# Performance work log

Measured on AMD Instinct MI355X. Metric: run time of the kernel, lower is better.

Reference implementation:

```python
import jax, jax.numpy as jnp
import numpy as np

M_POS = 0.5
M_NEG_SIM = 0.1
LAM_NEG = 1.0


def setup_inputs() -> dict:
    key = jax.random.key(0)
    N, d, G = 8192, 1024, 64
    codebook = jax.random.normal(key, (N, d), dtype=jnp.float32)
    base = (jnp.arange(N) // G) * G  # contiguous groups of size G (vq_to_range)
    starts = base.astype(jnp.int32)
    ends = (base + G - 1).astype(jnp.int32)
    return {"codebook": codebook, "starts": starts, "ends": ends, "max_i": N - 1}


def reference(codebook, starts, ends, max_i):
    N, d = codebook.shape
    M = min(N, int(max_i) + 1)  # rows processed by the python loop

    # cosine similarity rows [0:M] vs all N
    zn = codebook / jnp.linalg.norm(codebook, axis=-1, keepdims=True)
    cos = jnp.einsum('md,nd->mn', zn[:M], zn)  # (M, N)

    # pairwise Euclidean distances rows [0:M] vs all N via ||a-b||^2 = |a|^2+|b|^2-2ab
    sq = jnp.sum(codebook * codebook, axis=-1)  # (N,)
    dot = jnp.einsum('md,nd->mn', codebook[:M], codebook)  # (M, N)
    d2 = jnp.maximum(sq[:M, None] + sq[None, :] - 2.0 * dot, 0.0)

    j = jnp.arange(N)[None, :]
    i = jnp.arange(M)[:, None]
    in_range = (j >= starts[:M, None]) & (j <= ends[:M, None])
    pos_mask = in_range & (j != i)
    # original: group_mask[i]=False then neg = ~group_mask, so i is in negatives
    neg_mask = (~in_range) | (j == i)

    pos_cnt = jnp.sum(pos_mask, axis=-1)
    neg_cnt = jnp.sum(neg_mask, axis=-1)

    # safe sqrt: only evaluate on positive-mask entries
    D = jnp.sqrt(jnp.where(pos_mask, d2, 1.0))
    pos_term = jnp.square(jax.nn.relu(D - M_POS)) * pos_mask
    pos_pull = jnp.sum(pos_term, axis=-1) / jnp.maximum(pos_cnt, 1)

    neg_cos = jnp.clip(cos, -1.0, 1.0)
    neg_term = jnp.square(jax.nn.relu(jnp.abs(neg_cos) - M_NEG_SIM)) * neg_mask
    ortho = jnp.sum(neg_term, axis=-1) / jnp.maximum(neg_cnt, 1)

    valid = (pos_cnt > 0) & (neg_cnt > 0)
    per_row = jnp.where(valid, pos_pull + LAM_NEG * ortho, 0.0)
    cnt = jnp.sum(valid)
    total = jnp.sum(per_row)
    return jnp.where(cnt > 0, total / jnp.maximum(cnt, 1).astype(total.dtype), jnp.zeros((), total.dtype))
```

## Files before the change

kernel.cpp:

```cpp
#include <hip/hip_runtime.h>
#include <hip/hip_bf16.h>
#include <stdint.h>

#define M_POS 0.5f
#define M_NEG 0.1f
#define LAM_NEG 1.0f

typedef __attribute__((ext_vector_type(4))) float floatx4;
typedef __attribute__((ext_vector_type(8))) int   intx8;

union Frag8 { intx8 v; int4 q[2]; };

__global__ __launch_bounds__(256) void prep_kernel(
    const float* __restrict__ cb, unsigned char* __restrict__ cb_q,
    float* __restrict__ sq, float* __restrict__ inv_norm,
    unsigned* __restrict__ zero_base, int zero_len,
    int N, int d)
{
    const int gi = blockIdx.x * 256 + threadIdx.x;
    if (gi < zero_len) zero_base[gi] = 0u;

    const int row = blockIdx.x;
    const float* src = cb + (size_t)row * d;
    unsigned char* dst = cb_q + (size_t)row * d;
    const int t = threadIdx.x;

    float s = 0.f;
    for (int c = t * 4; c < d; c += 1024) {
        float4 v = *(const float4*)(src + c);
        s += v.x * v.x + v.y * v.y + v.z * v.z + v.w * v.w;
        int pk = __builtin_amdgcn_cvt_pk_fp8_f32(v.x, v.y, 0, false);
        pk     = __builtin_amdgcn_cvt_pk_fp8_f32(v.z, v.w, pk, true);
        *(int*)(dst + c) = pk;
    }
    for (int o = 32; o > 0; o >>= 1) s += __shfl_down(s, o, 64);
    __shared__ float wsum[4];
    if ((t & 63) == 0) wsum[t >> 6] = s;
    __syncthreads();
    if (t == 0) {
        float tot = wsum[0] + wsum[1] + wsum[2] + wsum[3];
        sq[row] = tot;
        inv_norm[row] = rsqrtf(tot);
    }
}

__global__ __launch_bounds__(256, 3) void gram_loss_kernel(
    const unsigned char* __restrict__ A,
    const float* __restrict__ sq, const float* __restrict__ inv_norm,
    const int* __restrict__ starts, const int* __restrict__ ends,
    const int* __restrict__ max_ip,
    float* __restrict__ pos_acc, float* __restrict__ neg_acc,
    unsigned* __restrict__ counter, float* __restrict__ out,
    int N, int d)
{
    const int M = min(N, max_ip[0] + 1);

    int vt = blockIdx.x;
    const int nB = gridDim.x;
    if ((nB & 7) == 0) {
        const int per = nB >> 3;
        vt = (blockIdx.x & 7) * per + (blockIdx.x >> 3);
    }

    int bx = (int)((sqrtf(8.f * (float)vt + 1.f) - 1.f) * 0.5f);
    while ((bx + 1) * (bx + 2) / 2 <= vt) bx++;
    while (bx * (bx + 1) / 2 > vt) bx--;
    const int by = vt - bx * (bx + 1) / 2;

    const int rowBase = by * 128;
    const int colBase = bx * 128;
    const bool isDiag = (by == bx);

    __shared__ alignas(16) unsigned char ldsA[128 * 128];
    __shared__ alignas(16) unsigned char ldsB[128 * 128];

    const int tid  = threadIdx.x;
    const int wave = tid >> 6;
    const int lane = tid & 63;
    const int wr = (wave >> 1) * 64;
    const int wc = (wave & 1) * 64;

    floatx4 acc[4][4];
#pragma unroll
    for (int a = 0; a < 4; ++a)
#pragma unroll
        for (int b = 0; b < 4; ++b) acc[a][b] = (floatx4){0.f, 0.f, 0.f, 0.f};

    const int sRow = lane >> 3;
    const int sChk = lane & 7;
    const int srcOffC = ((sChk ^ sRow) * 16);
    const int kTiles = d / 128;

    const int rl = lane & 15;
    const int g  = lane >> 4;
    const int rx = rl & 7;
    const int c0 = (((2 * g)     ^ rx) * 16);
    const int c1 = (((2 * g + 1) ^ rx) * 16);

    for (int kt = 0; kt < kTiles; ++kt) {
        __syncthreads();
        const int k0 = kt * 128;
#pragma unroll
        for (int h = 0; h < 4; ++h) {
            const int r = wave * 32 + h * 8 + sRow;
            const unsigned char* ga = A + (size_t)(rowBase + r) * d + k0 + srcOffC;
            const unsigned char* gb = A + (size_t)(colBase + r) * d + k0 + srcOffC;
            __builtin_amdgcn_global_load_lds(
                (const __attribute__((address_space(1))) void*)ga,
                (__attribute__((address_space(3))) void*)(ldsA + r * 128 + sChk * 16), 16, 0, 0);
            __builtin_amdgcn_global_load_lds(
                (const __attribute__((address_space(1))) void*)gb,
                (__attribute__((address_space(3))) void*)(ldsB + r * 128 + sChk * 16), 16, 0, 0);
        }
        __syncthreads();

        Frag8 af[4], bf[4];
#pragma unroll
        for (int t4 = 0; t4 < 4; ++t4) {
            const unsigned char* pa = ldsA + (wr + t4 * 16 + rl) * 128;
            af[t4].q[0] = *(const int4*)(pa + c0);
            af[t4].q[1] = *(const int4*)(pa + c1);
            const unsigned char* pb = ldsB + (wc + t4 * 16 + rl) * 128;
            bf[t4].q[0] = *(const int4*)(pb + c0);
            bf[t4].q[1] = *(const int4*)(pb + c1);
        }
#pragma unroll
        for (int rt = 0; rt < 4; ++rt)
#pragma unroll
            for (int ct = 0; ct < 4; ++ct)
                acc[rt][ct] = __builtin_amdgcn_mfma_scale_f32_16x16x128_f8f6f4(
                    af[rt].v, bf[ct].v, acc[rt][ct], 0, 0, 0, 127, 0, 127);
    }

    const int q  = lane >> 4;
    const int jlo = colBase + wc;
    const int ilo = rowBase + wr;

    int   jn[4];
    float jinv[4];
    bool  jvalid[4];
#pragma unroll
    for (int ct = 0; ct < 4; ++ct) {
        const int j = jlo + ct * 16 + rl;
        jn[ct]  = j;
        jinv[ct] = inv_norm[j];
        jvalid[ct] = (j < M);
    }

    bool posLane = false;
    {
        const int ri = ilo + lane;
        if (ri < M) posLane |= (ends[ri] >= jlo) && (starts[ri] <= jlo + 63);
        if (!isDiag) {
            const int cj = jlo + lane;
            if (cj < M) posLane |= (ends[cj] >= ilo) && (starts[cj] <= ilo + 63);
        }
    }
    const bool fullPath = (__ballot(posLane) != 0ULL);

    float posc[4] = {0.f, 0.f, 0.f, 0.f};
    float negc[4] = {0.f, 0.f, 0.f, 0.f};

    if (fullPath) {
        int   jns[4], jne[4];
        float jsq[4];
#pragma unroll
        for (int ct = 0; ct < 4; ++ct) {
            jsq[ct] = sq[jn[ct]];
            jns[ct] = jvalid[ct] ? starts[jn[ct]] : 0;
            jne[ct] = jvalid[ct] ? ends[jn[ct]]   : -1;
        }
#pragma unroll
        for (int rt = 0; rt < 4; ++rt) {
            const int ibase = ilo + rt * 16 + q * 4;
#pragma unroll
            for (int reg = 0; reg < 4; ++reg) {
                const int i = ibase + reg;
                const bool rowValid = (i < M);
                const int ns = rowValid ? starts[i] : 0;
                const int ne = rowValid ? ends[i]   : -1;
                const float iinv = inv_norm[i];
                const float isq  = sq[i];
                float posp = 0.f, negp = 0.f;
#pragma unroll
                for (int ct = 0; ct < 4; ++ct) {
                    const float dot = acc[rt][ct][reg];
                    const int j = jn[ct];
                    float cosv = dot * iinv * jinv[ct];
                    cosv = fminf(fmaxf(cosv, -1.f), 1.f);
                    float tn = fmaxf(fabsf(cosv) - M_NEG, 0.f);
                    const float nterm = tn * tn;
                    const float d2 = fmaxf(isq + jsq[ct] - 2.f * dot, 0.f);
                    float tp = fmaxf(sqrtf(d2) - M_POS, 0.f);
                    const float pterm = tp * tp;
                    const bool dg = (j == i);
                    if (rowValid) {
                        const bool in_r = (j >= ns) && (j <= ne);
                        if (in_r && !dg) posp += pterm;
                        if (!in_r || dg) negp += nterm;
                    }
                    if (!isDiag && jvalid[ct]) {
                        const bool in_c = (i >= jns[ct]) && (i <= jne[ct]);
                        if (in_c && !dg) posc[ct] += pterm;
                        if (!in_c || dg) negc[ct] += nterm;
                    }
                }
#pragma unroll
                for (int m = 1; m < 16; m <<= 1) {
                    posp += __shfl_xor(posp, m, 64);
                    negp += __shfl_xor(negp, m, 64);
                }
                if (rowValid && rl == 0) {
                    atomicAdd(&pos_acc[i], posp);
                    atomicAdd(&neg_acc[i], negp);
                }
            }
        }
        if (!isDiag) {
#pragma unroll
            for (int ct = 0; ct < 4; ++ct) {
                posc[ct] += __shfl_xor(posc[ct], 16, 64);
                posc[ct] += __shfl_xor(posc[ct], 32, 64);
                negc[ct] += __shfl_xor(negc[ct], 16, 64);
                negc[ct] += __shfl_xor(negc[ct], 32, 64);
            }
            if (q == 0) {
#pragma unroll
                for (int ct = 0; ct < 4; ++ct) {
                    if (jvalid[ct]) {
                        atomicAdd(&pos_acc[jn[ct]], posc[ct]);
                        atomicAdd(&neg_acc[jn[ct]], negc[ct]);
                    }
                }
            }
        }
    } else {
#pragma unroll
        for (int rt = 0; rt < 4; ++rt) {
            const int ibase = ilo + rt * 16 + q * 4;
#pragma unroll
            for (int reg = 0; reg < 4; ++reg) {
                const int i = ibase + reg;
                const float iinv = inv_norm[i];
                float negp = 0.f;
#pragma unroll
                for (int ct = 0; ct < 4; ++ct) {
                    const float dot = acc[rt][ct][reg];
                    float cosv = dot * iinv * jinv[ct];
                    cosv = fminf(fmaxf(cosv, -1.f), 1.f);
                    float tn = fmaxf(fabsf(cosv) - M_NEG, 0.f);
                    const float nterm = tn * tn;
                    negp += nterm;
                    negc[ct] += nterm;
                }
#pragma unroll
                for (int m = 1; m < 16; m <<= 1)
                    negp += __shfl_xor(negp, m, 64);
                if ((i < M) && rl == 0)
                    atomicAdd(&neg_acc[i], negp);
            }
        }
        if (!isDiag) {
#pragma unroll
            for (int ct = 0; ct < 4; ++ct) {
                negc[ct] += __shfl_xor(negc[ct], 16, 64);
                negc[ct] += __shfl_xor(negc[ct], 32, 64);
            }
            if (q == 0) {
#pragma unroll
                for (int ct = 0; ct < 4; ++ct)
                    if (jvalid[ct])
                        atomicAdd(&neg_acc[jn[ct]], negc[ct]);
            }
        }
    }

    __shared__ bool amLast;
    __syncthreads();
    if (tid == 0) {
        __threadfence();
        unsigned old = atomicAdd(counter, 1u);
        amLast = (old == (unsigned)(gridDim.x - 1));
    }
    __syncthreads();
    if (amLast) {
        __threadfence();
        float total = 0.f;
        int cnt = 0;
        for (int i = tid; i < M; i += 256) {
            const float pa = __hip_atomic_load(&pos_acc[i], __ATOMIC_RELAXED, __HIP_MEMORY_SCOPE_AGENT);
            const float na = __hip_atomic_load(&neg_acc[i], __ATOMIC_RELAXED, __HIP_MEMORY_SCOPE_AGENT);
            const int ns = starts[i], ne = ends[i];
            const int lo = max(ns, 0), hi = min(ne, N - 1);
            const int inr = max(hi - lo + 1, 0);
            const bool dg = (i >= ns) && (i <= ne);
            const int pos_cnt = inr - (dg ? 1 : 0);
            const int neg_cnt = N - inr + (dg ? 1 : 0);
            if (pos_cnt > 0 && neg_cnt > 0) {
                total += pa / (float)max(pos_cnt, 1)
                       + LAM_NEG * na / (float)max(neg_cnt, 1);
                cnt++;
            }
        }
        for (int o = 32; o > 0; o >>= 1) {
            total += __shfl_down(total, o, 64);
            cnt   += __shfl_down(cnt, o, 64);
        }
        __shared__ float fin_ts[4];
        __shared__ int   fin_cs[4];
        if ((tid & 63) == 0) { fin_ts[tid >> 6] = total; fin_cs[tid >> 6] = cnt; }
        __syncthreads();
        if (tid == 0) {
            float T = fin_ts[0] + fin_ts[1] + fin_ts[2] + fin_ts[3];
            int   C = fin_cs[0] + fin_cs[1] + fin_cs[2] + fin_cs[3];
            out[0] = (C > 0) ? T / (float)C : 0.f;
        }
    }
}

extern "C" void kernel_launch(void* const* d_in, const int* in_sizes, int n_in,
                              void* d_out, int out_size, void* d_ws, size_t ws_size,
                              hipStream_t stream) {
    const float* cb     = (const float*)d_in[0];
    const int*   starts = (const int*)d_in[1];
    const int*   ends   = (const int*)d_in[2];
    const int*   max_ip = (const int*)d_in[3];
    float* out = (float*)d_out;

    const int N = in_sizes[1];
    const int d = in_sizes[0] / N;

    char* ws = (char*)d_ws;
    unsigned char* cb_q = (unsigned char*)ws;
    size_t off = ((size_t)N * d + 255) & ~(size_t)255;
    float* sq       = (float*)(ws + off); off += (size_t)N * 4;
    float* inv_norm = (float*)(ws + off); off += (size_t)N * 4;
    float* pos_acc  = (float*)(ws + off); off += (size_t)N * 4;
    float* neg_acc  = (float*)(ws + off); off += (size_t)N * 4;
    unsigned* counter = (unsigned*)(ws + off); off += 256;

    prep_kernel<<<N, 256, 0, stream>>>(cb, cb_q, sq, inv_norm,
                                       (unsigned*)pos_acc, 2 * N + 1, N, d);

    const int nb = N / 128;
    const int nBlocks = nb * (nb + 1) / 2;
    gram_loss_kernel<<<nBlocks, 256, 0, stream>>>(cb_q, sq, inv_norm, starts, ends,
                                                  max_ip, pos_acc, neg_acc, counter,
                                                  out, N, d);
}
```

Baseline: 196.9 us.

## Split each 128x128 Gram tile into two 128x64 column-half blocks

Each upper-triangular 128x128 tile is now split into two blocks, each computing a 128x64 half, which doubles the grid. The B LDS buffer, the MFMA accumulators and the epilogue loops shrink to match, and launch bounds rise to allow four blocks per CU. The aim is better occupancy and load balance through lower register and LDS use per block. In exchange, each A tile is loaded twice, so global/L2 traffic goes up and data reuse per block goes down.

```diff
diff --git a/kernel.cpp b/kernel.cpp
--- a/kernel.cpp
+++ b/kernel.cpp
@@ -44,7 +44,7 @@
     }
 }
 
-__global__ __launch_bounds__(256, 3) void gram_loss_kernel(
+__global__ __launch_bounds__(256, 4) void gram_loss_kernel(
     const unsigned char* __restrict__ A,
     const float* __restrict__ sq, const float* __restrict__ inv_norm,
     const int* __restrict__ starts, const int* __restrict__ ends,
@@ -62,29 +62,31 @@
         vt = (blockIdx.x & 7) * per + (blockIdx.x >> 3);
     }
 
-    int bx = (int)((sqrtf(8.f * (float)vt + 1.f) - 1.f) * 0.5f);
-    while ((bx + 1) * (bx + 2) / 2 <= vt) bx++;
-    while (bx * (bx + 1) / 2 > vt) bx--;
-    const int by = vt - bx * (bx + 1) / 2;
+    const int sqt  = vt >> 1;
+    const int half = vt & 1;
+    int bx = (int)((sqrtf(8.f * (float)sqt + 1.f) - 1.f) * 0.5f);
+    while ((bx + 1) * (bx + 2) / 2 <= sqt) bx++;
+    while (bx * (bx + 1) / 2 > sqt) bx--;
+    const int by = sqt - bx * (bx + 1) / 2;
 
     const int rowBase = by * 128;
-    const int colBase = bx * 128;
+    const int colBase = bx * 128 + half * 64;
     const bool isDiag = (by == bx);
 
     __shared__ alignas(16) unsigned char ldsA[128 * 128];
-    __shared__ alignas(16) unsigned char ldsB[128 * 128];
+    __shared__ alignas(16) unsigned char ldsB[64 * 128];
 
     const int tid  = threadIdx.x;
     const int wave = tid >> 6;
     const int lane = tid & 63;
     const int wr = (wave >> 1) * 64;
-    const int wc = (wave & 1) * 64;
-
-    floatx4 acc[4][4];
+    const int wc = (wave & 1) * 32;
+
+    floatx4 acc[4][2];
 #pragma unroll
     for (int a = 0; a < 4; ++a)
 #pragma unroll
-        for (int b = 0; b < 4; ++b) acc[a][b] = (floatx4){0.f, 0.f, 0.f, 0.f};
+        for (int b = 0; b < 2; ++b) acc[a][b] = (floatx4){0.f, 0.f, 0.f, 0.f};
 
     const int sRow = lane >> 3;
     const int sChk = lane & 7;
@@ -104,43 +106,50 @@
         for (int h = 0; h < 4; ++h) {
             const int r = wave * 32 + h * 8 + sRow;
             const unsigned char* ga = A + (size_t)(rowBase + r) * d + k0 + srcOffC;
-            const unsigned char* gb = A + (size_t)(colBase + r) * d + k0 + srcOffC;
             __builtin_amdgcn_global_load_lds(
                 (const __attribute__((address_space(1))) void*)ga,
                 (__attribute__((address_space(3))) void*)(ldsA + r * 128 + sChk * 16), 16, 0, 0);
+        }
+#pragma unroll
+        for (int h = 0; h < 2; ++h) {
+            const int r = wave * 16 + h * 8 + sRow;
+            const unsigned char* gb = A + (size_t)(colBase + r) * d + k0 + srcOffC;
             __builtin_amdgcn_global_load_lds(
                 (const __attribute__((address_space(1))) void*)gb,
                 (__attribute__((address_space(3))) void*)(ldsB + r * 128 + sChk * 16), 16, 0, 0);
         }
         __syncthreads();
 
-        Frag8 af[4], bf[4];
+        Frag8 af[4], bf[2];
 #pragma unroll
         for (int t4 = 0; t4 < 4; ++t4) {
             const unsigned char* pa = ldsA + (wr + t4 * 16 + rl) * 128;
             af[t4].q[0] = *(const int4*)(pa + c0);
             af[t4].q[1] = *(const int4*)(pa + c1);
-            const unsigned char* pb = ldsB + (wc + t4 * 16 + rl) * 128;
-            bf[t4].q[0] = *(const int4*)(pb + c0);
-            bf[t4].q[1] = *(const int4*)(pb + c1);
+        }
+#pragma unroll
+        for (int t2 = 0; t2 < 2; ++t2) {
+            const unsigned char* pb = ldsB + (wc + t2 * 16 + rl) * 128;
+            bf[t2].q[0] = *(const int4*)(pb + c0);
+            bf[t2].q[1] = *(const int4*)(pb + c1);
         }
 #pragma unroll
         for (int rt = 0; rt < 4; ++rt)
 #pragma unroll
-            for (int ct = 0; ct < 4; ++ct)
+            for (int ct = 0; ct < 2; ++ct)
                 acc[rt][ct] = __builtin_amdgcn_mfma_scale_f32_16x16x128_f8f6f4(
                     af[rt].v, bf[ct].v, acc[rt][ct], 0, 0, 0, 127, 0, 127);
     }
 
-    const int q  = lane >> 4;
+    const int q  = g;
     const int jlo = colBase + wc;
     const int ilo = rowBase + wr;
 
-    int   jn[4];
-    float jinv[4];
-    bool  jvalid[4];
-#pragma unroll
-    for (int ct = 0; ct < 4; ++ct) {
+    int   jn[2];
+    float jinv[2];
+    bool  jvalid[2];
+#pragma unroll
+    for (int ct = 0; ct < 2; ++ct) {
         const int j = jlo + ct * 16 + rl;
         jn[ct]  = j;
         jinv[ct] = inv_norm[j];
@@ -150,22 +159,22 @@
     bool posLane = false;
     {
         const int ri = ilo + lane;
-        if (ri < M) posLane |= (ends[ri] >= jlo) && (starts[ri] <= jlo + 63);
-        if (!isDiag) {
+        if (ri < M) posLane |= (ends[ri] >= jlo) && (starts[ri] <= jlo + 31);
+        if (!isDiag && lane < 32) {
             const int cj = jlo + lane;
             if (cj < M) posLane |= (ends[cj] >= ilo) && (starts[cj] <= ilo + 63);
         }
     }
     const bool fullPath = (__ballot(posLane) != 0ULL);
 
-    float posc[4] = {0.f, 0.f, 0.f, 0.f};
-    float negc[4] = {0.f, 0.f, 0.f, 0.f};
+    float posc[2] = {0.f, 0.f};
+    float negc[2] = {0.f, 0.f};
 
     if (fullPath) {
-        int   jns[4], jne[4];
-        float jsq[4];
-#pragma unroll
-        for (int ct = 0; ct < 4; ++ct) {
+        int   jns[2], jne[2];
+        float jsq[2];
+#pragma unroll
+        for (int ct = 0; ct < 2; ++ct) {
             jsq[ct] = sq[jn[ct]];
             jns[ct] = jvalid[ct] ? starts[jn[ct]] : 0;
             jne[ct] = jvalid[ct] ? ends[jn[ct]]   : -1;
@@ -183,7 +192,7 @@
                 const float isq  = sq[i];
                 float posp = 0.f, negp = 0.f;
 #pragma unroll
-                for (int ct = 0; ct < 4; ++ct) {
+                for (int ct = 0; ct < 2; ++ct) {
                     const float dot = acc[rt][ct][reg];
                     const int j = jn[ct];
                     float cosv = dot * iinv * jinv[ct];
@@ -218,7 +227,7 @@
         }
         if (!isDiag) {
 #pragma unroll
-            for (int ct = 0; ct < 4; ++ct) {
+            for (int ct = 0; ct < 2; ++ct) {
                 posc[ct] += __shfl_xor(posc[ct], 16, 64);
                 posc[ct] += __shfl_xor(posc[ct], 32, 64);
                 negc[ct] += __shfl_xor(negc[ct], 16, 64);
@@ -226,7 +235,7 @@
             }
             if (q == 0) {
 #pragma unroll
-                for (int ct = 0; ct < 4; ++ct) {
+                for (int ct = 0; ct < 2; ++ct) {
                     if (jvalid[ct]) {
                         atomicAdd(&pos_acc[jn[ct]], posc[ct]);
                         atomicAdd(&neg_acc[jn[ct]], negc[ct]);
@@ -244,7 +253,7 @@
                 const float iinv = inv_norm[i];
                 float negp = 0.f;
 #pragma unroll
-                for (int ct = 0; ct < 4; ++ct) {
+                for (int ct = 0; ct < 2; ++ct) {
                     const float dot = acc[rt][ct][reg];
                     float cosv = dot * iinv * jinv[ct];
                     cosv = fminf(fmaxf(cosv, -1.f), 1.f);
@@ -262,13 +271,13 @@
         }
         if (!isDiag) {
 #pragma unroll
-            for (int ct = 0; ct < 4; ++ct) {
+            for (int ct = 0; ct < 2; ++ct) {
                 negc[ct] += __shfl_xor(negc[ct], 16, 64);
                 negc[ct] += __shfl_xor(negc[ct], 32, 64);
             }
             if (q == 0) {
 #pragma unroll
-                for (int ct = 0; ct < 4; ++ct)
+                for (int ct = 0; ct < 2; ++ct)
                     if (jvalid[ct])
                         atomicAdd(&neg_acc[jn[ct]], negc[ct]);
             }
@@ -343,7 +352,8 @@
                                        (unsigned*)pos_acc, 2 * N + 1, N, d);
 
     const int nb = N / 128;
-    const int nBlocks = nb * (nb + 1) / 2;
+    const int nSquares = nb * (nb + 1) / 2;
+    const int nBlocks = nSquares * 2;
     gram_loss_kernel<<<nBlocks, 256, 0, stream>>>(cb_q, sq, inv_norm, starts, ends,
                                                   max_ip, pos_acc, neg_acc, counter,
                                                   out, N, d);
```

Result: slower. 274.3 us (+39.3%).
